# Optimization experiments

Hardware: AMD Instinct MI355X
Metric: run time of the kernel (lower is better)

Reference implementation:

```python
import jax, jax.numpy as jnp
import numpy as np

HIDDEN = 2048
HEADS = 16
HEAD_DIM = HIDDEN // HEADS          # 128
LATENT = HIDDEN // 4                # 512
ROPE_DIM = HEAD_DIM // 2            # 64 (dim passed to LlamaRotaryEmbedding)
B, S = 2, 2048
SCALE = 1.0 / np.sqrt(HEAD_DIM)


def _linear_params(key, d_in, d_out):
    kw, kb = jax.random.split(key)
    bound = 1.0 / np.sqrt(d_in)
    W = jax.random.uniform(kw, (d_in, d_out), jnp.float32, -bound, bound)
    b = jax.random.uniform(kb, (d_out,), jnp.float32, -bound, bound)
    return W, b


def _rope_tables(seq_len):
    # inv_freq over arange(0, ROPE_DIM, 2) -> ROPE_DIM//2 frequencies
    inv_freq = 1.0 / (10000.0 ** (np.arange(0, ROPE_DIM, 2, dtype=np.float32) / ROPE_DIM))
    t = np.arange(seq_len, dtype=np.float32)
    freqs = np.einsum('i,j->ij', t, inv_freq)  # [S, ROPE_DIM//2]
    return jnp.asarray(np.cos(freqs)), jnp.asarray(np.sin(freqs))


def setup_inputs() -> dict:
    key = jax.random.key(0)
    ks = jax.random.split(key, 10)
    x = jax.random.normal(ks[0], (B, S, HIDDEN), jnp.float32)
    # causal mask: 1 where attending allowed, 0 above the diagonal
    attention_mask = jnp.tril(jnp.ones((S, S), jnp.int32))[None].repeat(B, axis=0)
    W_kv_d, b_kv_d = _linear_params(ks[1], HIDDEN, LATENT)
    W_q_d, b_q_d = _linear_params(ks[2], HIDDEN, LATENT)
    W_k_u, b_k_u = _linear_params(ks[3], LATENT, HIDDEN // 2)
    W_q_u, b_q_u = _linear_params(ks[4], LATENT, HIDDEN // 2)
    W_v_u, b_v_u = _linear_params(ks[5], LATENT, HIDDEN)
    W_rk, b_rk = _linear_params(ks[6], HIDDEN, HIDDEN // 2)
    W_rq, b_rq = _linear_params(ks[7], LATENT, HIDDEN // 2)
    W_o, b_o = _linear_params(ks[8], HIDDEN, HIDDEN)
    return dict(x=x, attention_mask=attention_mask,
                W_kv_d=W_kv_d, b_kv_d=b_kv_d, W_q_d=W_q_d, b_q_d=b_q_d,
                W_k_u=W_k_u, b_k_u=b_k_u, W_q_u=W_q_u, b_q_u=b_q_u,
                W_v_u=W_v_u, b_v_u=b_v_u, W_rk=W_rk, b_rk=b_rk,
                W_rq=W_rq, b_rq=b_rq, W_o=W_o, b_o=b_o)


def _apply_rope(xr, cos, sin):
    # xr: [B,S,H,ROPE_DIM]; cos/sin: [S, ROPE_DIM//2]
    half = xr.shape[-1] // 2
    rot, pas = xr[..., :half], xr[..., half:]
    c = cos[None, :, None, :]
    s = sin[None, :, None, :]
    return jnp.concatenate([rot * c - pas * s, rot * s + pas * c], axis=-1)


def reference(x, attention_mask, W_kv_d, b_kv_d, W_q_d, b_q_d, W_k_u, b_k_u,
              W_q_u, b_q_u, W_v_u, b_v_u, W_rk, b_rk, W_rq, b_rq, W_o, b_o):
    Bsz, seq, _ = x.shape
    cos, sin = _rope_tables(seq)
    kv_d = x @ W_kv_d + b_kv_d                      # [B,S,latent]
    q_d = x @ W_q_d + b_q_d                         # [B,S,latent]
    k1 = (kv_d @ W_k_u + b_k_u).reshape(Bsz, seq, HEADS, HEAD_DIM // 2)
    q1 = (q_d @ W_q_u + b_q_u).reshape(Bsz, seq, HEADS, HEAD_DIM // 2)
    v = (kv_d @ W_v_u + b_v_u).reshape(Bsz, seq, HEADS, HEAD_DIM)
    k2 = (x @ W_rk + b_rk).reshape(Bsz, seq, HEADS, HEAD_DIM // 2)
    q2 = (q_d @ W_rq + b_rq).reshape(Bsz, seq, HEADS, HEAD_DIM // 2)
    k2 = _apply_rope(k2, cos, sin)
    q2 = _apply_rope(q2, cos, sin)
    k = jnp.concatenate([k1, k2], axis=-1)          # [B,S,H,head_dim]
    q = jnp.concatenate([q1, q2], axis=-1)
    scores = jnp.einsum('bqhd,bkhd->bhqk', q, k) * SCALE
    scores = jnp.where(attention_mask[:, None, :, :] == 0, -jnp.inf, scores)
    attn = jax.nn.softmax(scores, axis=-1)
    out = jnp.einsum('bhqk,bkhd->bqhd', attn, v).reshape(Bsz, seq, HIDDEN)
    return out @ W_o + b_o
```

## Files before the change

kernel.cpp:

```cpp
#include <hip/hip_runtime.h>
#include <hip/hip_bf16.h>
#include <math.h>

#define HIDDEN 2048
#define HEADS 16
#define HEAD_DIM 128
#define LATENT 512
#define SEQ 2048
#define BATCH 2
#define MROWS (BATCH*SEQ)
#define ATTN_SCALE 0.08838834764831845f

typedef unsigned short u16;
typedef __hip_bfloat16 bf16;
typedef __attribute__((ext_vector_type(8))) short bf16x8;
typedef __attribute__((ext_vector_type(4))) float f32x4;

__device__ inline float bf2f(u16 u) { return __uint_as_float(((unsigned)u) << 16); }
__device__ inline short f2bf_s(float v) { bf16 t = __float2bfloat16(v); return *(short*)&t; }

#define GLOAD_LDS(gp, lp) \
    __builtin_amdgcn_global_load_lds((const __attribute__((address_space(1))) unsigned int*)(gp), \
                                     (__attribute__((address_space(3))) unsigned int*)(lp), 16, 0, 0)

__global__ void rope_table_kernel(float* __restrict__ cosT, float* __restrict__ sinT) {
    int gid = blockIdx.x * blockDim.x + threadIdx.x;
    if (gid >= SEQ * 32) return;
    int t = gid >> 5, j = gid & 31;
    float inv = powf(10000.0f, -(float)j * (1.0f / 32.0f));
    float ang = (float)t * inv;
    cosT[gid] = cosf(ang);
    sinT[gid] = sinf(ang);
}

__global__ __launch_bounds__(256) void castx_kernel(const float* __restrict__ x, bf16* __restrict__ xb) {
    size_t gid = (size_t)blockIdx.x * 256 + threadIdx.x;
    const float* p = x + gid * 8;
    float4 a = *(const float4*)p;
    float4 b = *(const float4*)(p + 4);
    bf16 o[8] = {__float2bfloat16(a.x), __float2bfloat16(a.y), __float2bfloat16(a.z), __float2bfloat16(a.w),
                 __float2bfloat16(b.x), __float2bfloat16(b.y), __float2bfloat16(b.z), __float2bfloat16(b.w)};
    *(uint4*)(xb + gid * 8) = *(uint4*)o;
}

__global__ __launch_bounds__(256) void tcast_kernel(const float* __restrict__ W, bf16* __restrict__ Wt,
                                                    int K, int N) {
    __shared__ float T[32][33];
    int k0 = blockIdx.x * 32, n0 = blockIdx.y * 32;
    int tx = threadIdx.x & 31, ty = threadIdx.x >> 5;
#pragma unroll
    for (int p = 0; p < 4; p++) {
        int kr = p * 8 + ty;
        T[kr][tx] = W[(size_t)(k0 + kr) * N + n0 + tx];
    }
    __syncthreads();
#pragma unroll
    for (int p = 0; p < 4; p++) {
        int nr = p * 8 + ty;
        Wt[(size_t)(n0 + nr) * K + k0 + tx] = __float2bfloat16(T[tx][nr]);
    }
}

template<int FUSE>
__global__ __launch_bounds__(256) void mfma_gemm(
    const bf16* __restrict__ A, const bf16* __restrict__ Bt,
    const float* __restrict__ bias0, const float* __restrict__ bias1, const float* __restrict__ bias2,
    void* __restrict__ d0, void* __restrict__ d1, void* __restrict__ d2,
    const float* __restrict__ cosT, const float* __restrict__ sinT,
    int M, int N, int K)
{
    constexpr int BM = 128, BN = 128, BK = 32;
    __shared__ __align__(16) short As[2][BM * BK];
    __shared__ __align__(16) short Bs[2][BN * BK];

    const int tid = threadIdx.x;
    const int wid = tid >> 6;
    const int lane = tid & 63;
    const int wm = (wid >> 1) * 64;
    const int wn = (wid & 1) * 64;
    const int bm = blockIdx.y * BM, bn = blockIdx.x * BN;
    const int fr = lane & 15;
    const int fk = lane >> 4;

    const int srowA = wid * 32 + (lane >> 2);
    const int scol = (lane & 3) * 8;

    f32x4 acc[4][4];
#pragma unroll
    for (int mi = 0; mi < 4; mi++)
#pragma unroll
        for (int ni = 0; ni < 4; ni++)
            acc[mi][ni] = (f32x4){0.f, 0.f, 0.f, 0.f};

    const int NT = K / BK;
#pragma unroll
    for (int i = 0; i < 2; i++) {
        GLOAD_LDS(A + (size_t)(bm + srowA + i * 16) * K + scol, &As[0][(wid * 32 + i * 16) * BK]);
        GLOAD_LDS(Bt + (size_t)(bn + srowA + i * 16) * K + scol, &Bs[0][(wid * 32 + i * 16) * BK]);
    }

    int cur = 0;
    for (int t = 0; t < NT; t++) {
        __syncthreads();
        if (t + 1 < NT) {
            size_t kk = (size_t)(t + 1) * BK;
#pragma unroll
            for (int i = 0; i < 2; i++) {
                GLOAD_LDS(A + (size_t)(bm + srowA + i * 16) * K + kk + scol, &As[cur ^ 1][(wid * 32 + i * 16) * BK]);
                GLOAD_LDS(Bt + (size_t)(bn + srowA + i * 16) * K + kk + scol, &Bs[cur ^ 1][(wid * 32 + i * 16) * BK]);
            }
        }
        bf16x8 af[4], bfr[4];
#pragma unroll
        for (int mi = 0; mi < 4; mi++)
            af[mi] = *(const bf16x8*)&As[cur][(wm + mi * 16 + fr) * BK + fk * 8];
#pragma unroll
        for (int ni = 0; ni < 4; ni++)
            bfr[ni] = *(const bf16x8*)&Bs[cur][(wn + ni * 16 + fr) * BK + fk * 8];
#pragma unroll
        for (int mi = 0; mi < 4; mi++)
#pragma unroll
            for (int ni = 0; ni < 4; ni++)
                acc[mi][ni] = __builtin_amdgcn_mfma_f32_16x16x32_bf16(af[mi], bfr[ni], acc[mi][ni], 0, 0, 0);
        cur ^= 1;
    }

    const int cr = (lane >> 4) * 4;
#pragma unroll
    for (int mi = 0; mi < 4; mi++) {
#pragma unroll
        for (int j = 0; j < 4; j++) {
            int m = bm + wm + mi * 16 + cr + j;
            int bb = m >> 11;
            int s = m & 2047;

            if constexpr (FUSE == 4) {
#pragma unroll
                for (int ni = 0; ni < 4; ni++) {
                    int n = bn + wn + ni * 16 + fr;
                    ((float*)d0)[(size_t)m * N + n] = acc[mi][ni][j] + bias0[n];
                }
            } else if constexpr (FUSE == 1) {
                if (bn < 512) {
#pragma unroll
                    for (int ni = 0; ni < 4; ni++) {
                        int n = bn + wn + ni * 16 + fr;
                        ((bf16*)d0)[(size_t)m * 512 + n] = __float2bfloat16(acc[mi][ni][j] + bias0[n]);
                    }
                } else if (bn < 1024) {
#pragma unroll
                    for (int ni = 0; ni < 4; ni++) {
                        int n = bn + wn + ni * 16 + fr - 512;
                        ((bf16*)d1)[(size_t)m * 512 + n] = __float2bfloat16(acc[mi][ni][j] + bias1[n]);
                    }
                } else {
#pragma unroll
                    for (int ni = 0; ni < 2; ni++) {
                        int nl = bn + wn + ni * 16 + fr - 1024;
                        int hh = nl >> 6, dd = nl & 63;
                        float rot = acc[mi][ni][j] + bias2[nl];
                        float pas = acc[mi][ni + 2][j] + bias2[nl + 32];
                        float c = cosT[s * 32 + dd], sn = sinT[s * 32 + dd];
                        bf16* o = (bf16*)d2 + ((size_t)(bb * HEADS + hh) * SEQ + s) * HEAD_DIM + 64 + dd;
                        o[0]  = __float2bfloat16(rot * c - pas * sn);
                        o[32] = __float2bfloat16(rot * sn + pas * c);
                    }
                }
            } else if constexpr (FUSE == 2) {
                if (bn < 1024) {
#pragma unroll
                    for (int ni = 0; ni < 4; ni++) {
                        int nl = bn + wn + ni * 16 + fr;
                        int hh = nl >> 6, dd = nl & 63;
                        ((bf16*)d0)[((size_t)(bb * HEADS + hh) * SEQ + s) * HEAD_DIM + dd] =
                            __float2bfloat16(acc[mi][ni][j] + bias0[nl]);
                    }
                } else {
#pragma unroll
                    for (int ni = 0; ni < 4; ni++) {
                        int nl = bn + wn + ni * 16 + fr - 1024;
                        int hh = nl >> 7, dd = nl & 127;
                        ((bf16*)d1)[((size_t)(bb * HEADS + hh) * HEAD_DIM + dd) * SEQ + s] =
                            __float2bfloat16(acc[mi][ni][j] + bias1[nl]);
                    }
                }
            } else {
                if (bn < 1024) {
#pragma unroll
                    for (int ni = 0; ni < 4; ni++) {
                        int nl = bn + wn + ni * 16 + fr;
                        int hh = nl >> 6, dd = nl & 63;
                        ((bf16*)d0)[((size_t)(bb * HEADS + hh) * SEQ + s) * HEAD_DIM + dd] =
                            __float2bfloat16((acc[mi][ni][j] + bias0[nl]) * ATTN_SCALE);
                    }
                } else {
#pragma unroll
                    for (int ni = 0; ni < 2; ni++) {
                        int nl = bn + wn + ni * 16 + fr - 1024;
                        int hh = nl >> 6, dd = nl & 63;
                        float rot = (acc[mi][ni][j] + bias1[nl]) * ATTN_SCALE;
                        float pas = (acc[mi][ni + 2][j] + bias1[nl + 32]) * ATTN_SCALE;
                        float c = cosT[s * 32 + dd], sn = sinT[s * 32 + dd];
                        bf16* o = (bf16*)d1 + ((size_t)(bb * HEADS + hh) * SEQ + s) * HEAD_DIM + 64 + dd;
                        o[0]  = __float2bfloat16(rot * c - pas * sn);
                        o[32] = __float2bfloat16(rot * sn + pas * c);
                    }
                }
            }
        }
    }
}

__global__ __launch_bounds__(256) void attn_mfma_kernel(
    const bf16* __restrict__ qg, const bf16* __restrict__ kg,
    const bf16* __restrict__ vtg, bf16* __restrict__ outp)
{
    const int f = blockIdx.x;
    const int xcd = f & 7, slot = f >> 3;
    const int g = xcd * 4 + (slot >> 4);
    const int pid = slot & 15;
    const int b = g >> 4, h = g & 15;

    const int tid = threadIdx.x;
    const int w = tid >> 6, lane = tid & 63;
    const int fr = lane & 15, fq = lane >> 4;
    const int r7 = fr & 7;

    const bf16* Q  = qg  + (size_t)(b * HEADS + h) * SEQ * HEAD_DIM;
    const bf16* K  = kg  + (size_t)(b * HEADS + h) * SEQ * HEAD_DIM;
    const bf16* Vt = vtg + (size_t)(b * HEADS + h) * HEAD_DIM * SEQ;

    __shared__ __align__(16) short Ks[2][64 * 128];
    __shared__ __align__(16) short Vs[2][128 * 64];
    __shared__ __align__(16) short Ps[64 * 64];

    const int krow = tid >> 4;
    const int kch  = tid & 15;
    const int vrow = tid >> 3;
    const int vch  = tid & 7;

#pragma unroll 1
    for (int seg = 0; seg < 2; seg++) {
        const int qt = seg ? (31 - pid) : pid;
        const int q0 = qt * 64;
        const int qrow = q0 + w * 16 + fr;

        bf16x8 qf[4];
#pragma unroll
        for (int kk = 0; kk < 4; kk++)
            qf[kk] = *(const bf16x8*)(Q + (size_t)(q0 + w * 16 + fr) * HEAD_DIM + kk * 32 + fq * 8);

        f32x4 accO[8];
#pragma unroll
        for (int ci = 0; ci < 8; ci++) accO[ci] = (f32x4){0.f, 0.f, 0.f, 0.f};
        float m_run = -INFINITY, l_run = 0.f;

        __syncthreads();
#pragma unroll
        for (int p = 0; p < 4; p++) {
            int rK = krow + p * 16;
            GLOAD_LDS(K + (size_t)rK * HEAD_DIM + ((kch ^ (rK & 7)) * 8), &Ks[0][rK * 128 + kch * 8]);
            int rV = vrow + p * 32;
            GLOAD_LDS(Vt + (size_t)rV * SEQ + ((vch ^ (rV & 7)) * 8), &Vs[0][rV * 64 + vch * 8]);
        }

        int cur = 0;
        for (int kt = 0; kt <= qt; kt++) {
            __syncthreads();
            if (kt < qt) {
#pragma unroll
                for (int p = 0; p < 4; p++) {
                    int rK = krow + p * 16;
                    GLOAD_LDS(K + (size_t)((kt + 1) * 64 + rK) * HEAD_DIM + ((kch ^ (rK & 7)) * 8),
                              &Ks[cur ^ 1][rK * 128 + kch * 8]);
                    int rV = vrow + p * 32;
                    GLOAD_LDS(Vt + (size_t)rV * SEQ + (kt + 1) * 64 + ((vch ^ (rV & 7)) * 8),
                              &Vs[cur ^ 1][rV * 64 + vch * 8]);
                }
            }

            f32x4 accS[4];
#pragma unroll
            for (int ni = 0; ni < 4; ni++) accS[ni] = (f32x4){0.f, 0.f, 0.f, 0.f};
#pragma unroll
            for (int kk = 0; kk < 4; kk++) {
#pragma unroll
                for (int ni = 0; ni < 4; ni++) {
                    bf16x8 kf = *(const bf16x8*)&Ks[cur][(ni * 16 + fr) * 128 + (((kk * 4 + fq) ^ r7) * 8)];
                    accS[ni] = __builtin_amdgcn_mfma_f32_16x16x32_bf16(kf, qf[kk], accS[ni], 0, 0, 0);
                }
            }

            const bool diag = (kt == qt);
            float pv[16];
            float mloc = -INFINITY;
#pragma unroll
            for (int ni = 0; ni < 4; ni++)
#pragma unroll
                for (int reg = 0; reg < 4; reg++) {
                    float sc = accS[ni][reg];
                    int key = kt * 64 + ni * 16 + fq * 4 + reg;
                    if (diag && key > qrow) sc = -INFINITY;
                    pv[ni * 4 + reg] = sc;
                    mloc = fmaxf(mloc, sc);
                }
            mloc = fmaxf(mloc, __shfl_xor(mloc, 16));
            mloc = fmaxf(mloc, __shfl_xor(mloc, 32));
            float mn = fmaxf(m_run, mloc);
            float rs = __expf(m_run - mn);
            m_run = mn;
            float sum = 0.f;
#pragma unroll
            for (int i = 0; i < 16; i++) {
                float p = __expf(pv[i] - mn);
                pv[i] = p;
                sum += p;
            }
            sum += __shfl_xor(sum, 16);
            sum += __shfl_xor(sum, 32);
            l_run = l_run * rs + sum;

            if (__any(rs < 1.0f)) {
                float rsb[4];
#pragma unroll
                for (int reg = 0; reg < 4; reg++) rsb[reg] = __shfl(rs, fq * 4 + reg);
#pragma unroll
                for (int ci = 0; ci < 8; ci++)
#pragma unroll
                    for (int reg = 0; reg < 4; reg++)
                        accO[ci][reg] *= rsb[reg];
            }

#pragma unroll
            for (int ni = 0; ni < 4; ni++) {
                unsigned lo = (unsigned)(u16)f2bf_s(pv[ni * 4 + 0]) | ((unsigned)(u16)f2bf_s(pv[ni * 4 + 1]) << 16);
                unsigned hi = (unsigned)(u16)f2bf_s(pv[ni * 4 + 2]) | ((unsigned)(u16)f2bf_s(pv[ni * 4 + 3]) << 16);
                uint2 u; u.x = lo; u.y = hi;
                *(uint2*)&Ps[(w * 16 + fr) * 64 + (((2 * ni + (fq >> 1)) ^ r7) * 8) + (fq & 1) * 4] = u;
            }

#pragma unroll
            for (int kk = 0; kk < 2; kk++) {
                bf16x8 pf = *(const bf16x8*)&Ps[(w * 16 + fr) * 64 + (((kk * 4 + fq) ^ r7) * 8)];
#pragma unroll
                for (int ci = 0; ci < 8; ci++) {
                    bf16x8 vf = *(const bf16x8*)&Vs[cur][(ci * 16 + fr) * 64 + (((kk * 4 + fq) ^ r7) * 8)];
                    accO[ci] = __builtin_amdgcn_mfma_f32_16x16x32_bf16(pf, vf, accO[ci], 0, 0, 0);
                }
            }
            cur ^= 1;
        }

        float linv = 1.0f / l_run;
#pragma unroll
        for (int reg = 0; reg < 4; reg++) {
            float invb = __shfl(linv, fq * 4 + reg);
            bf16* dst = outp + ((size_t)(b * SEQ) + q0 + w * 16 + fq * 4 + reg) * HIDDEN + h * HEAD_DIM + fr;
#pragma unroll
            for (int ci = 0; ci < 8; ci++)
                dst[ci * 16] = __float2bfloat16(accO[ci][reg] * invb);
        }
    }
}

extern "C" void kernel_launch(void* const* d_in, const int* in_sizes, int n_in,
                              void* d_out, int out_size, void* d_ws, size_t ws_size,
                              hipStream_t stream)
{
    const float* x      = (const float*)d_in[0];
    const float* W_kv_d = (const float*)d_in[2];
    const float* b_kv_d = (const float*)d_in[3];
    const float* W_q_d  = (const float*)d_in[4];
    const float* b_q_d  = (const float*)d_in[5];
    const float* W_k_u  = (const float*)d_in[6];
    const float* b_k_u  = (const float*)d_in[7];
    const float* W_q_u  = (const float*)d_in[8];
    const float* b_q_u  = (const float*)d_in[9];
    const float* W_v_u  = (const float*)d_in[10];
    const float* b_v_u  = (const float*)d_in[11];
    const float* W_rk   = (const float*)d_in[12];
    const float* b_rk   = (const float*)d_in[13];
    const float* W_rq   = (const float*)d_in[14];
    const float* b_rq   = (const float*)d_in[15];
    const float* W_o    = (const float*)d_in[16];
    const float* b_o    = (const float*)d_in[17];

    float* cosT = (float*)d_ws;
    float* sinT = cosT + SEQ * 32;
    bf16* kv_d  = (bf16*)(sinT + SEQ * 32);
    bf16* q_d   = kv_d + (size_t)MROWS * LATENT;
    bf16* qg    = q_d + (size_t)MROWS * LATENT;
    bf16* kg    = qg + (size_t)BATCH * HEADS * SEQ * HEAD_DIM;
    bf16* vtg   = kg + (size_t)BATCH * HEADS * SEQ * HEAD_DIM;
    bf16* attnb = vtg + (size_t)BATCH * HEADS * SEQ * HEAD_DIM;
    bf16* xb    = attnb + (size_t)MROWS * HIDDEN;
    bf16* Wt_g1 = xb + (size_t)MROWS * HIDDEN;
    bf16* Wt_g2 = Wt_g1 + (size_t)2048 * HIDDEN;
    bf16* Wt_g3 = Wt_g2 + (size_t)3072 * LATENT;
    bf16* Wt_o  = Wt_g3 + (size_t)2048 * LATENT;

    rope_table_kernel<<<(SEQ * 32 + 255) / 256, 256, 0, stream>>>(cosT, sinT);
    castx_kernel<<<MROWS * HIDDEN / 8 / 256, 256, 0, stream>>>(x, xb);
    tcast_kernel<<<dim3(HIDDEN / 32, LATENT / 32), 256, 0, stream>>>(W_kv_d, Wt_g1, HIDDEN, LATENT);
    tcast_kernel<<<dim3(HIDDEN / 32, LATENT / 32), 256, 0, stream>>>(W_q_d, Wt_g1 + (size_t)512 * HIDDEN, HIDDEN, LATENT);
    tcast_kernel<<<dim3(HIDDEN / 32, 1024 / 32), 256, 0, stream>>>(W_rk, Wt_g1 + (size_t)1024 * HIDDEN, HIDDEN, 1024);
    tcast_kernel<<<dim3(LATENT / 32, 1024 / 32), 256, 0, stream>>>(W_k_u, Wt_g2, LATENT, 1024);
    tcast_kernel<<<dim3(LATENT / 32, HIDDEN / 32), 256, 0, stream>>>(W_v_u, Wt_g2 + (size_t)1024 * LATENT, LATENT, HIDDEN);
    tcast_kernel<<<dim3(LATENT / 32, 1024 / 32), 256, 0, stream>>>(W_q_u, Wt_g3, LATENT, 1024);
    tcast_kernel<<<dim3(LATENT / 32, 1024 / 32), 256, 0, stream>>>(W_rq, Wt_g3 + (size_t)1024 * LATENT, LATENT, 1024);
    tcast_kernel<<<dim3(HIDDEN / 32, HIDDEN / 32), 256, 0, stream>>>(W_o, Wt_o, HIDDEN, HIDDEN);

    mfma_gemm<1><<<dim3(2048 / 128, MROWS / 128), 256, 0, stream>>>(
        xb, Wt_g1, b_kv_d, b_q_d, b_rk, kv_d, q_d, kg, cosT, sinT, MROWS, 2048, HIDDEN);
    mfma_gemm<2><<<dim3(3072 / 128, MROWS / 128), 256, 0, stream>>>(
        kv_d, Wt_g2, b_k_u, b_v_u, nullptr, kg, vtg, nullptr, nullptr, nullptr, MROWS, 3072, LATENT);
    mfma_gemm<3><<<dim3(2048 / 128, MROWS / 128), 256, 0, stream>>>(
        q_d, Wt_g3, b_q_u, b_rq, nullptr, qg, qg, nullptr, cosT, sinT, MROWS, 2048, LATENT);

    attn_mfma_kernel<<<512, 256, 0, stream>>>(qg, kg, vtg, attnb);

    mfma_gemm<4><<<dim3(2048 / 128, MROWS / 128), 256, 0, stream>>>(
        attnb, Wt_o, b_o, nullptr, nullptr, d_out, nullptr, nullptr, nullptr, nullptr, MROWS, 2048, HIDDEN);
}
```

Measured before the change: 271.8 us.

## Merge prep kernels, fuse up-projection GEMMs, fold log2e into Q scale

All preprocessing launches (rope tables, x cast, eight weight transpose-casts) are merged into one prep kernel that dispatches on block index. The K/V and Q up-projection GEMMs become a single launch that picks its A operand per column block, raising grid size and removing a launch. The softmax switches from expf to exp2f by folding log2(e) into the Q scale. Together these aim to cut launch overhead and tail effects, at the cost of branchier kernels and a changed weight workspace layout.

```diff
diff --git a/kernel.cpp b/kernel.cpp
--- a/kernel.cpp
+++ b/kernel.cpp
@@ -10,6 +10,7 @@
 #define BATCH 2
 #define MROWS (BATCH*SEQ)
 #define ATTN_SCALE 0.08838834764831845f
+#define QSCALE (0.08838834764831845f * 1.4426950408889634f)
 
 typedef unsigned short u16;
 typedef __hip_bfloat16 bf16;
@@ -23,31 +24,53 @@
     __builtin_amdgcn_global_load_lds((const __attribute__((address_space(1))) unsigned int*)(gp), \
                                      (__attribute__((address_space(3))) unsigned int*)(lp), 16, 0, 0)
 
-__global__ void rope_table_kernel(float* __restrict__ cosT, float* __restrict__ sinT) {
-    int gid = blockIdx.x * blockDim.x + threadIdx.x;
-    if (gid >= SEQ * 32) return;
-    int t = gid >> 5, j = gid & 31;
-    float inv = powf(10000.0f, -(float)j * (1.0f / 32.0f));
-    float ang = (float)t * inv;
-    cosT[gid] = cosf(ang);
-    sinT[gid] = sinf(ang);
-}
-
-__global__ __launch_bounds__(256) void castx_kernel(const float* __restrict__ x, bf16* __restrict__ xb) {
-    size_t gid = (size_t)blockIdx.x * 256 + threadIdx.x;
-    const float* p = x + gid * 8;
-    float4 a = *(const float4*)p;
-    float4 b = *(const float4*)(p + 4);
-    bf16 o[8] = {__float2bfloat16(a.x), __float2bfloat16(a.y), __float2bfloat16(a.z), __float2bfloat16(a.w),
-                 __float2bfloat16(b.x), __float2bfloat16(b.y), __float2bfloat16(b.z), __float2bfloat16(b.w)};
-    *(uint4*)(xb + gid * 8) = *(uint4*)o;
-}
-
-__global__ __launch_bounds__(256) void tcast_kernel(const float* __restrict__ W, bf16* __restrict__ Wt,
-                                                    int K, int N) {
+__global__ __launch_bounds__(256) void prep_kernel(
+    const float* __restrict__ x, bf16* __restrict__ xb,
+    const float* __restrict__ W_kv_d, const float* __restrict__ W_q_d, const float* __restrict__ W_rk,
+    const float* __restrict__ W_k_u, const float* __restrict__ W_v_u,
+    const float* __restrict__ W_q_u, const float* __restrict__ W_rq, const float* __restrict__ W_o,
+    bf16* __restrict__ Wt_g1, bf16* __restrict__ Wt_g2, bf16* __restrict__ Wt_o,
+    float* __restrict__ cosT, float* __restrict__ sinT)
+{
+    const int tid = threadIdx.x;
+    int r = blockIdx.x;
+
+    if (r < 256) {
+        int gid = r * 256 + tid;
+        int t = gid >> 5, j = gid & 31;
+        float inv = powf(10000.0f, -(float)j * (1.0f / 32.0f));
+        float ang = (float)t * inv;
+        cosT[gid] = cosf(ang);
+        sinT[gid] = sinf(ang);
+        return;
+    }
+    r -= 256;
+    if (r < 4096) {
+        size_t gid = (size_t)r * 256 + tid;
+        const float* p = x + gid * 8;
+        float4 a = *(const float4*)p;
+        float4 b = *(const float4*)(p + 4);
+        bf16 o[8] = {__float2bfloat16(a.x), __float2bfloat16(a.y), __float2bfloat16(a.z), __float2bfloat16(a.w),
+                     __float2bfloat16(b.x), __float2bfloat16(b.y), __float2bfloat16(b.z), __float2bfloat16(b.w)};
+        *(uint4*)(xb + gid * 8) = *(uint4*)o;
+        return;
+    }
+    r -= 4096;
+
+    const float* W; bf16* Wt; int K, N;
+    if (r < 1024)            { W = W_kv_d; Wt = Wt_g1;                        K = 2048; N = 512;  }
+    else if (r < 2048)       { r -= 1024; W = W_q_d; Wt = Wt_g1 + (size_t)512 * 2048;  K = 2048; N = 512;  }
+    else if (r < 4096)       { r -= 2048; W = W_rk;  Wt = Wt_g1 + (size_t)1024 * 2048; K = 2048; N = 1024; }
+    else if (r < 4608)       { r -= 4096; W = W_k_u; Wt = Wt_g2;                       K = 512;  N = 1024; }
+    else if (r < 5632)       { r -= 4608; W = W_v_u; Wt = Wt_g2 + (size_t)1024 * 512;  K = 512;  N = 2048; }
+    else if (r < 6144)       { r -= 5632; W = W_q_u; Wt = Wt_g2 + (size_t)3072 * 512;  K = 512;  N = 1024; }
+    else if (r < 6656)       { r -= 6144; W = W_rq;  Wt = Wt_g2 + (size_t)4096 * 512;  K = 512;  N = 1024; }
+    else                     { r -= 6656; W = W_o;   Wt = Wt_o;                        K = 2048; N = 2048; }
+
+    const int kb = r % (K / 32), nb = r / (K / 32);
+    const int k0 = kb * 32, n0 = nb * 32;
     __shared__ float T[32][33];
-    int k0 = blockIdx.x * 32, n0 = blockIdx.y * 32;
-    int tx = threadIdx.x & 31, ty = threadIdx.x >> 5;
+    const int tx = tid & 31, ty = tid >> 5;
 #pragma unroll
     for (int p = 0; p < 4; p++) {
         int kr = p * 8 + ty;
@@ -63,8 +86,9 @@
 
 template<int FUSE>
 __global__ __launch_bounds__(256) void mfma_gemm(
-    const bf16* __restrict__ A, const bf16* __restrict__ Bt,
-    const float* __restrict__ bias0, const float* __restrict__ bias1, const float* __restrict__ bias2,
+    const bf16* __restrict__ A, const bf16* __restrict__ A2, const bf16* __restrict__ Bt,
+    const float* __restrict__ bias0, const float* __restrict__ bias1,
+    const float* __restrict__ bias2, const float* __restrict__ bias3,
     void* __restrict__ d0, void* __restrict__ d1, void* __restrict__ d2,
     const float* __restrict__ cosT, const float* __restrict__ sinT,
     int M, int N, int K)
@@ -85,6 +109,9 @@
     const int srowA = wid * 32 + (lane >> 2);
     const int scol = (lane & 3) * 8;
 
+    const bf16* Abase = A;
+    if constexpr (FUSE == 23) { if (bn >= 3072) Abase = A2; }
+
     f32x4 acc[4][4];
 #pragma unroll
     for (int mi = 0; mi < 4; mi++)
@@ -95,7 +122,7 @@
     const int NT = K / BK;
 #pragma unroll
     for (int i = 0; i < 2; i++) {
-        GLOAD_LDS(A + (size_t)(bm + srowA + i * 16) * K + scol, &As[0][(wid * 32 + i * 16) * BK]);
+        GLOAD_LDS(Abase + (size_t)(bm + srowA + i * 16) * K + scol, &As[0][(wid * 32 + i * 16) * BK]);
         GLOAD_LDS(Bt + (size_t)(bn + srowA + i * 16) * K + scol, &Bs[0][(wid * 32 + i * 16) * BK]);
     }
 
@@ -106,7 +133,7 @@
             size_t kk = (size_t)(t + 1) * BK;
 #pragma unroll
             for (int i = 0; i < 2; i++) {
-                GLOAD_LDS(A + (size_t)(bm + srowA + i * 16) * K + kk + scol, &As[cur ^ 1][(wid * 32 + i * 16) * BK]);
+                GLOAD_LDS(Abase + (size_t)(bm + srowA + i * 16) * K + kk + scol, &As[cur ^ 1][(wid * 32 + i * 16) * BK]);
                 GLOAD_LDS(Bt + (size_t)(bn + srowA + i * 16) * K + kk + scol, &Bs[cur ^ 1][(wid * 32 + i * 16) * BK]);
             }
         }
@@ -166,7 +193,7 @@
                         o[32] = __float2bfloat16(rot * sn + pas * c);
                     }
                 }
-            } else if constexpr (FUSE == 2) {
+            } else {
                 if (bn < 1024) {
 #pragma unroll
                     for (int ni = 0; ni < 4; ni++) {
@@ -175,7 +202,7 @@
                         ((bf16*)d0)[((size_t)(bb * HEADS + hh) * SEQ + s) * HEAD_DIM + dd] =
                             __float2bfloat16(acc[mi][ni][j] + bias0[nl]);
                     }
-                } else {
+                } else if (bn < 3072) {
 #pragma unroll
                     for (int ni = 0; ni < 4; ni++) {
                         int nl = bn + wn + ni * 16 + fr - 1024;
@@ -183,25 +210,23 @@
                         ((bf16*)d1)[((size_t)(bb * HEADS + hh) * HEAD_DIM + dd) * SEQ + s] =
                             __float2bfloat16(acc[mi][ni][j] + bias1[nl]);
                     }
-                }
-            } else {
-                if (bn < 1024) {
+                } else if (bn < 4096) {
 #pragma unroll
                     for (int ni = 0; ni < 4; ni++) {
-                        int nl = bn + wn + ni * 16 + fr;
+                        int nl = bn + wn + ni * 16 + fr - 3072;
                         int hh = nl >> 6, dd = nl & 63;
-                        ((bf16*)d0)[((size_t)(bb * HEADS + hh) * SEQ + s) * HEAD_DIM + dd] =
-                            __float2bfloat16((acc[mi][ni][j] + bias0[nl]) * ATTN_SCALE);
+                        ((bf16*)d2)[((size_t)(bb * HEADS + hh) * SEQ + s) * HEAD_DIM + dd] =
+                            __float2bfloat16((acc[mi][ni][j] + bias2[nl]) * QSCALE);
                     }
                 } else {
 #pragma unroll
                     for (int ni = 0; ni < 2; ni++) {
-                        int nl = bn + wn + ni * 16 + fr - 1024;
+                        int nl = bn + wn + ni * 16 + fr - 4096;
                         int hh = nl >> 6, dd = nl & 63;
-                        float rot = (acc[mi][ni][j] + bias1[nl]) * ATTN_SCALE;
-                        float pas = (acc[mi][ni + 2][j] + bias1[nl + 32]) * ATTN_SCALE;
+                        float rot = (acc[mi][ni][j] + bias3[nl]) * QSCALE;
+                        float pas = (acc[mi][ni + 2][j] + bias3[nl + 32]) * QSCALE;
                         float c = cosT[s * 32 + dd], sn = sinT[s * 32 + dd];
-                        bf16* o = (bf16*)d1 + ((size_t)(bb * HEADS + hh) * SEQ + s) * HEAD_DIM + 64 + dd;
+                        bf16* o = (bf16*)d2 + ((size_t)(bb * HEADS + hh) * SEQ + s) * HEAD_DIM + 64 + dd;
                         o[0]  = __float2bfloat16(rot * c - pas * sn);
                         o[32] = __float2bfloat16(rot * sn + pas * c);
                     }
@@ -307,12 +332,12 @@
             mloc = fmaxf(mloc, __shfl_xor(mloc, 16));
             mloc = fmaxf(mloc, __shfl_xor(mloc, 32));
             float mn = fmaxf(m_run, mloc);
-            float rs = __expf(m_run - mn);
+            float rs = exp2f(m_run - mn);
             m_run = mn;
             float sum = 0.f;
 #pragma unroll
             for (int i = 0; i < 16; i++) {
-                float p = __expf(pv[i] - mn);
+                float p = exp2f(pv[i] - mn);
                 pv[i] = p;
                 sum += p;
             }
@@ -396,29 +421,20 @@
     bf16* xb    = attnb + (size_t)MROWS * HIDDEN;
     bf16* Wt_g1 = xb + (size_t)MROWS * HIDDEN;
     bf16* Wt_g2 = Wt_g1 + (size_t)2048 * HIDDEN;
-    bf16* Wt_g3 = Wt_g2 + (size_t)3072 * LATENT;
-    bf16* Wt_o  = Wt_g3 + (size_t)2048 * LATENT;
-
-    rope_table_kernel<<<(SEQ * 32 + 255) / 256, 256, 0, stream>>>(cosT, sinT);
-    castx_kernel<<<MROWS * HIDDEN / 8 / 256, 256, 0, stream>>>(x, xb);
-    tcast_kernel<<<dim3(HIDDEN / 32, LATENT / 32), 256, 0, stream>>>(W_kv_d, Wt_g1, HIDDEN, LATENT);
-    tcast_kernel<<<dim3(HIDDEN / 32, LATENT / 32), 256, 0, stream>>>(W_q_d, Wt_g1 + (size_t)512 * HIDDEN, HIDDEN, LATENT);
-    tcast_kernel<<<dim3(HIDDEN / 32, 1024 / 32), 256, 0, stream>>>(W_rk, Wt_g1 + (size_t)1024 * HIDDEN, HIDDEN, 1024);
-    tcast_kernel<<<dim3(LATENT / 32, 1024 / 32), 256, 0, stream>>>(W_k_u, Wt_g2, LATENT, 1024);
-    tcast_kernel<<<dim3(LATENT / 32, HIDDEN / 32), 256, 0, stream>>>(W_v_u, Wt_g2 + (size_t)1024 * LATENT, LATENT, HIDDEN);
-    tcast_kernel<<<dim3(LATENT / 32, 1024 / 32), 256, 0, stream>>>(W_q_u, Wt_g3, LATENT, 1024);
-    tcast_kernel<<<dim3(LATENT / 32, 1024 / 32), 256, 0, stream>>>(W_rq, Wt_g3 + (size_t)1024 * LATENT, LATENT, 1024);
-    tcast_kernel<<<dim3(HIDDEN / 32, HIDDEN / 32), 256, 0, stream>>>(W_o, Wt_o, HIDDEN, HIDDEN);
+    bf16* Wt_o  = Wt_g2 + (size_t)5120 * LATENT;
+
+    prep_kernel<<<15104, 256, 0, stream>>>(
+        x, xb, W_kv_d, W_q_d, W_rk, W_k_u, W_v_u, W_q_u, W_rq, W_o,
+        Wt_g1, Wt_g2, Wt_o, cosT, sinT);
 
     mfma_gemm<1><<<dim3(2048 / 128, MROWS / 128), 256, 0, stream>>>(
-        xb, Wt_g1, b_kv_d, b_q_d, b_rk, kv_d, q_d, kg, cosT, sinT, MROWS, 2048, HIDDEN);
-    mfma_gemm<2><<<dim3(3072 / 128, MROWS / 128), 256, 0, stream>>>(
-        kv_d, Wt_g2, b_k_u, b_v_u, nullptr, kg, vtg, nullptr, nullptr, nullptr, MROWS, 3072, LATENT);
-    mfma_gemm<3><<<dim3(2048 / 128, MROWS / 128), 256, 0, stream>>>(
-        q_d, Wt_g3, b_q_u, b_rq, nullptr, qg, qg, nullptr, cosT, sinT, MROWS, 2048, LATENT);
+        xb, nullptr, Wt_g1, b_kv_d, b_q_d, b_rk, nullptr, kv_d, q_d, kg, cosT, sinT, MROWS, 2048, HIDDEN);
+
+    mfma_gemm<23><<<dim3(5120 / 128, MROWS / 128), 256, 0, stream>>>(
+        kv_d, q_d, Wt_g2, b_k_u, b_v_u, b_q_u, b_rq, kg, vtg, qg, cosT, sinT, MROWS, 5120, LATENT);
 
     attn_mfma_kernel<<<512, 256, 0, stream>>>(qg, kg, vtg, attnb);
 
     mfma_gemm<4><<<dim3(2048 / 128, MROWS / 128), 256, 0, stream>>>(
-        attnb, Wt_o, b_o, nullptr, nullptr, d_out, nullptr, nullptr, nullptr, nullptr, MROWS, 2048, HIDDEN);
+        attnb, nullptr, Wt_o, b_o, nullptr, nullptr, nullptr, d_out, nullptr, nullptr, nullptr, nullptr, MROWS, 2048, HIDDEN);
 }
```

Result: faster. 261.9 us (-3.6%).
